# Kernel optimization log

Hardware: AMD Instinct MI355X
Metric: run time of the kernel (lower is better)

The kernel has to match this reference:

```python
import jax, jax.numpy as jnp
import numpy as np


def conv2d(x, w, pad=1):
    return jax.lax.conv_general_dilated(
        x, w, (1, 1), [(pad, pad), (pad, pad)],
        dimension_numbers=('NCHW', 'OIHW', 'NCHW'))


def bn(x, g, b, m, v, eps=1e-5):
    inv = g / jnp.sqrt(v + eps)
    return x * inv[None, :, None, None] + (b - m * inv)[None, :, None, None]


def deform_conv(x, wp, bp, wd):
    # v2-style DeformConv2D: internal p_conv -> offsets, bilinear sample, 3x3 conv
    b, c, h, w = x.shape
    ks = 3
    N = ks * ks
    offset = conv2d(x, wp, 1) + bp[None, :, None, None]   # (b, 2N, h, w)
    xp = jnp.pad(x, ((0, 0), (0, 0), (1, 1), (1, 1)))     # zero_padding(1)
    Hp, Wp = h + 2, w + 2
    off = offset.transpose(0, 2, 3, 1)                    # (b, h, w, 2N)
    pn_y, pn_x = jnp.meshgrid(jnp.arange(-1, 2), jnp.arange(-1, 2), indexing='ij')
    # sampling locations p = p_0 + p_n + offset (in padded coords)
    py = jnp.arange(1, h + 1)[None, :, None, None] + pn_y.reshape(-1)[None, None, None, :] + off[..., :N]
    px = jnp.arange(1, w + 1)[None, None, :, None] + pn_x.reshape(-1)[None, None, None, :] + off[..., N:]
    fy = jnp.floor(jax.lax.stop_gradient(py))
    fx = jnp.floor(jax.lax.stop_gradient(px))
    qy0 = jnp.clip(fy, 0, Hp - 1); qy1 = jnp.clip(fy + 1, 0, Hp - 1)
    qx0 = jnp.clip(fx, 0, Wp - 1); qx1 = jnp.clip(fx + 1, 0, Wp - 1)
    py = jnp.clip(py, 0, Hp - 1); px = jnp.clip(px, 0, Wp - 1)
    g_lt = (1 + (qy0 - py)) * (1 + (qx0 - px))
    g_rb = (1 - (qy1 - py)) * (1 - (qx1 - px))
    g_lb = (1 + (qy0 - py)) * (1 - (qx1 - px))
    g_rt = (1 - (qy1 - py)) * (1 + (qx0 - px))
    flat = xp.reshape(b, c, Hp * Wp)

    def gather(qy, qx):
        idx = (qy * Wp + qx).astype(jnp.int32).reshape(b, 1, -1)
        return jnp.take_along_axis(flat, idx, axis=2).reshape(b, c, h, w, N)

    x_off = (g_lt[:, None] * gather(qy0, qx0) + g_rb[:, None] * gather(qy1, qx1)
             + g_lb[:, None] * gather(qy0, qx1) + g_rt[:, None] * gather(qy1, qx0))
    outc = wd.shape[0]
    # equivalent to _reshape_x_offset + Conv2d(kernel=ks, stride=ks)
    return jnp.einsum('bchwn,ocn->bohw', x_off, wd.reshape(outc, c, N))


def setup_inputs() -> dict:
    key = jax.random.key(0)
    ks = jax.random.split(key, 24)
    B, H, W = 256, 28, 28

    def nrm(k, s, sc=1.0):
        return jax.random.normal(k, s, jnp.float32) * sc

    return {
        'x': nrm(ks[0], (B, 3, H, W)),
        'w1': nrm(ks[1], (32, 3, 3, 3), 0.2),
        'g1': jax.random.uniform(ks[2], (32,), jnp.float32) + 0.5,
        'b1': nrm(ks[3], (32,), 0.1),
        'm1': nrm(ks[4], (32,), 0.1),
        'v1': jax.random.uniform(ks[5], (32,), jnp.float32) + 0.5,
        'wp': nrm(ks[6], (18, 32, 3, 3), 0.01),  # p_conv: small offsets
        'bp': nrm(ks[7], (18,), 0.1),
        'w2': nrm(ks[8], (32, 32, 3, 3), 0.1),
        'g2': jax.random.uniform(ks[9], (32,), jnp.float32) + 0.5,
        'b2': nrm(ks[10], (32,), 0.1),
        'm2': nrm(ks[11], (32,), 0.1),
        'v2': jax.random.uniform(ks[12], (32,), jnp.float32) + 0.5,
        'w3': nrm(ks[13], (64, 32, 3, 3), 0.1),
        'g3': jax.random.uniform(ks[14], (64,), jnp.float32) + 0.5,
        'b3': nrm(ks[15], (64,), 0.1),
        'm3': nrm(ks[16], (64,), 0.1),
        'v3': jax.random.uniform(ks[17], (64,), jnp.float32) + 0.5,
        'wc': nrm(ks[18], (10, 64), 0.1),
        'bc': nrm(ks[19], (10,), 0.1),
    }


def reference(x, w1, g1, b1, m1, v1, wp, bp, w2, g2, b2, m2, v2,
              w3, g3, b3, m3, v3, wc, bc):
    h = bn(jax.nn.relu(conv2d(x, w1)), g1, b1, m1, v1)
    h = bn(jax.nn.relu(deform_conv(h, wp, bp, w2)), g2, b2, m2, v2)
    h = bn(jax.nn.relu(conv2d(h, w3)), g3, b3, m3, v3)
    h = h.mean(axis=(2, 3))               # avg_pool2d(28) on 28x28 -> global mean
    logits = h @ wc.T + bc
    return jax.nn.log_softmax(logits, axis=1)
```

## Files before the change

### kernel.cpp

```cpp
#include <hip/hip_runtime.h>
#include <hip/hip_bf16.h>
#include <math.h>

typedef __attribute__((ext_vector_type(8))) short short8;
typedef __attribute__((ext_vector_type(8))) _Float16 half8;
typedef __attribute__((ext_vector_type(4))) float floatx4;

#define NB 256
#define NW 16
#define NT (NW * 64)

#define WPB_OFF 0u
#define W2B_OFF 18432u
#define W3B_OFF 36864u
#define W1B_OFF 73728u
#define C1S_OFF 75776u
#define C2S_OFF 75904u
#define C3S_OFF 76032u

#define L_IMG1 0
#define L_U    50240
#define L_OFFT 100480
#define L_WL   125056
#define L_TOT  162944

static __device__ __forceinline__ unsigned short f2h(float f) {
    _Float16 h = (_Float16)f;
    unsigned short u;
    __builtin_memcpy(&u, &h, 2);
    return u;
}
static __device__ __forceinline__ float h2f(unsigned short u) {
    _Float16 h;
    __builtin_memcpy(&h, &u, 2);
    return (float)h;
}

static __device__ __forceinline__ unsigned pkh(float a, float b) {
    _Float16 ha = (_Float16)a, hb = (_Float16)b;
    unsigned short ua, ub;
    __builtin_memcpy(&ua, &ha, 2);
    __builtin_memcpy(&ub, &hb, 2);
    return (unsigned)ua | ((unsigned)ub << 16);
}

static __device__ __forceinline__ half8 h8(uint4 u) {
    half8 r;
    __builtin_memcpy(&r, &u, 16);
    return r;
}

static __device__ __forceinline__ unsigned pkmul_l(unsigned a, unsigned b) {
    unsigned d;
    asm("v_pk_mul_f16 %0, %1, %2 op_sel:[0,0] op_sel_hi:[0,1]"
        : "=v"(d) : "v"(a), "v"(b));
    return d;
}
static __device__ __forceinline__ unsigned pkfma_l(unsigned a, unsigned b, unsigned c) {
    unsigned d;
    asm("v_pk_fma_f16 %0, %1, %2, %3 op_sel:[0,0,0] op_sel_hi:[0,1,1]"
        : "=v"(d) : "v"(a), "v"(b), "v"(c));
    return d;
}
static __device__ __forceinline__ unsigned pkfma_h(unsigned a, unsigned b, unsigned c) {
    unsigned d;
    asm("v_pk_fma_f16 %0, %1, %2, %3 op_sel:[1,0,0] op_sel_hi:[1,1,1]"
        : "=v"(d) : "v"(a), "v"(b), "v"(c));
    return d;
}

__global__ void wcvt(const float* __restrict__ wp, const float* __restrict__ w2,
                     const float* __restrict__ w3, const float* __restrict__ w1,
                     const float* __restrict__ g1, const float* __restrict__ b1,
                     const float* __restrict__ m1, const float* __restrict__ v1,
                     const float* __restrict__ g2, const float* __restrict__ b2,
                     const float* __restrict__ m2, const float* __restrict__ v2,
                     const float* __restrict__ g3, const float* __restrict__ b3,
                     const float* __restrict__ m3, const float* __restrict__ v3,
                     unsigned short* __restrict__ wpb, unsigned short* __restrict__ w2b,
                     unsigned short* __restrict__ w3b, unsigned short* __restrict__ w1b,
                     float* __restrict__ c1s, float* __restrict__ c2s,
                     float* __restrict__ c3s)
{
    int t = blockIdx.x * 256 + threadIdx.x;
    if (t < 9216) {
        int oc = t / 288, k = t % 288;
        int n = k >> 5, ic = k & 31;
        wpb[t] = (oc < 18) ? f2h(wp[oc * 288 + ic * 9 + n]) : (unsigned short)0;
    } else if (t < 18432) {
        int i = t - 9216;
        int oc = i / 288, k = i % 288;
        int n = k >> 5, ic = k & 31;
        float inv = g2[oc] * rsqrtf(v2[oc] + 1e-5f);
        w2b[i] = f2h(w2[oc * 288 + ic * 9 + n] * inv);
    } else if (t < 36864) {
        int i = t - 18432;
        int oc = i / 288, k = i % 288;
        int n = k >> 5, ic = k & 31;
        float inv = g3[oc] * rsqrtf(v3[oc] + 1e-5f);
        w3b[i] = f2h(w3[oc * 288 + ic * 9 + n] * inv);
    } else if (t < 37888) {
        int i = t - 36864;
        int oc = i >> 5, k = i & 31;
        int n = k / 3, ic = k - n * 3;
        float inv = g1[oc] * rsqrtf(v1[oc] + 1e-5f);
        w1b[i] = (k < 27) ? f2h(w1[oc * 27 + ic * 9 + n] * inv) : (unsigned short)0;
    } else if (t < 37920) {
        int c = t - 37888;
        float inv = g1[c] * rsqrtf(v1[c] + 1e-5f);
        c1s[c] = b1[c] - m1[c] * inv;
    } else if (t < 37952) {
        int c = t - 37920;
        float inv = g2[c] * rsqrtf(v2[c] + 1e-5f);
        c2s[c] = b2[c] - m2[c] * inv;
    } else if (t < 38016) {
        int c = t - 37952;
        float inv = g3[c] * rsqrtf(v3[c] + 1e-5f);
        c3s[c] = b3[c] - m3[c] * inv;
    }
}

__global__ __launch_bounds__(NT, 4) void meganet(
    const float* __restrict__ x,
    const unsigned short* __restrict__ wpb, const unsigned short* __restrict__ w2b,
    const unsigned short* __restrict__ w3b, const unsigned short* __restrict__ w1b,
    const float* __restrict__ c1s, const float* __restrict__ c2s,
    const float* __restrict__ c3s, const float* __restrict__ bp,
    const float* __restrict__ wc, const float* __restrict__ bc,
    float* __restrict__ outp)
{
    __shared__ __align__(16) unsigned char ALL[L_TOT];
    int t = threadIdx.x, b = blockIdx.x;
    int w = t >> 6, l = t & 63, col = l & 15, q = l >> 4;

    unsigned char* img1 = ALL + L_IMG1;
    unsigned char* uimg = ALL + L_U;

    {
        const float4* xg = (const float4*)(x + (size_t)b * 2352);
        float4* xl = (float4*)uimg;
        for (int i = t; i < 588; i += NT) xl[i] = xg[i];
    }
    {
        const uint4* s1 = (const uint4*)wpb;
        const uint4* s2 = (const uint4*)w2b;
        for (int i = t; i < 2304; i += NT) {
            int row = i / 36, g = i - row * 36;
            uint4 v = (row < 32) ? s1[row * 36 + g] : s2[(row - 32) * 36 + g];
            *(uint4*)(ALL + L_WL + row * 592 + g * 16) = v;
        }
        if (t < 128) *(uint4*)(ALL + L_OFFT + t * 16) = ((const uint4*)w1b)[t];
    }
    if (t == 700) ((float*)uimg)[2352] = 0.f;
    if (t < 4)  *(uint4*)(img1 + 784 * 64 + t * 16) = make_uint4(0u, 0u, 0u, 0u);
    if (t >= 4 && t < 8) *(uint4*)(uimg + 784 * 64 + (t - 4) * 16) = make_uint4(0u, 0u, 0u, 0u);

    float s0 = c1s[col], s1v = c1s[16 + col];
    float bias0 = bp[col];
    float bias1 = (col < 2) ? bp[16 + col] : 0.f;
    float sh0 = c2s[col], sh1 = c2s[16 + col];

    __syncthreads();

    {
        half8 bf0 = h8(*(const uint4*)(ALL + L_OFFT + col * 64 + q * 16));
        half8 bf1 = h8(*(const uint4*)(ALL + L_OFFT + (16 + col) * 64 + q * 16));
        const float* xs = (const float*)uimg;
        for (int mt = w; mt < 49; mt += NW) {
            int p = mt * 16 + col;
            int y = p / 28, xx = p % 28;
            unsigned au[4];
#pragma unroll
            for (int jp = 0; jp < 4; jp++) {
                float vv[2];
#pragma unroll
                for (int h = 0; h < 2; h++) {
                    int k = q * 8 + jp * 2 + h;
                    int n = k / 3, ic = k - n * 3;
                    int yy = y + n / 3 - 1, xc = xx + n % 3 - 1;
                    bool ok = (k < 27) && ((unsigned)yy < 28u) && ((unsigned)xc < 28u);
                    int idx = ok ? (ic * 784 + yy * 28 + xc) : 2352;
                    vv[h] = xs[idx];
                }
                au[jp] = pkh(vv[0], vv[1]);
            }
            uint4 a4 = make_uint4(au[0], au[1], au[2], au[3]);
            half8 a = h8(a4);
            floatx4 d0 = {0.f, 0.f, 0.f, 0.f}, d1 = {0.f, 0.f, 0.f, 0.f};
            d0 = __builtin_amdgcn_mfma_f32_16x16x32_f16(a, bf0, d0, 0, 0, 0);
            d1 = __builtin_amdgcn_mfma_f32_16x16x32_f16(a, bf1, d1, 0, 0, 0);
#pragma unroll
            for (int r = 0; r < 4; r++) {
                int pout = mt * 16 + q * 4 + r;
                *(unsigned short*)(img1 + pout * 64 + col * 2) = f2h(fmaxf(d0[r], 0.f) + s0);
                *(unsigned short*)(img1 + pout * 64 + 32 + col * 2) = f2h(fmaxf(d1[r], 0.f) + s1v);
            }
        }
    }
    __syncthreads();

    {
        const unsigned char* ib = img1;
        unsigned char* wsc = ALL + L_OFFT + w * 1536;
        unsigned short* otw = (unsigned short*)wsc;
        unsigned char* gscr = wsc + 576;

        half8 b2fr[18];
#pragma unroll
        for (int n = 0; n < 9; n++) {
            b2fr[n]     = h8(*(const uint4*)(ALL + L_WL + (32 + col) * 592 + n * 64 + q * 16));
            b2fr[9 + n] = h8(*(const uint4*)(ALL + L_WL + (48 + col) * 592 + n * 64 + q * 16));
        }

        for (int mt = w; mt < 49; mt += NW) {
            int p = mt * 16 + col;
            int y = p / 28, xx = p % 28;

            floatx4 a0 = {0.f, 0.f, 0.f, 0.f}, a1 = {0.f, 0.f, 0.f, 0.f};
#pragma unroll
            for (int n = 0; n < 9; n++) {
                int yy = y + n / 3 - 1, xc = xx + n % 3 - 1;
                bool ok = ((unsigned)yy < 28u) && ((unsigned)xc < 28u);
                int tp = ok ? (yy * 28 + xc) : 784;
                half8 a  = h8(*(const uint4*)(ib + tp * 64 + q * 16));
                half8 p0 = h8(*(const uint4*)(ALL + L_WL + col * 592 + n * 64 + q * 16));
                half8 p1 = h8(*(const uint4*)(ALL + L_WL + (16 + col) * 592 + n * 64 + q * 16));
                a0 = __builtin_amdgcn_mfma_f32_16x16x32_f16(a, p0, a0, 0, 0, 0);
                a1 = __builtin_amdgcn_mfma_f32_16x16x32_f16(a, p1, a1, 0, 0, 0);
            }
#pragma unroll
            for (int r = 0; r < 4; r++)
                otw[(q * 4 + r) * 18 + col] = f2h(a0[r] + bias0);
            if (col < 2) {
#pragma unroll
                for (int r = 0; r < 4; r++)
                    otw[(q * 4 + r) * 18 + 16 + col] = f2h(a1[r] + bias1);
            }
            __asm__ volatile("s_waitcnt lgkmcnt(0)" ::: "memory");

            floatx4 d0 = {0.f, 0.f, 0.f, 0.f}, d1 = {0.f, 0.f, 0.f, 0.f};
#pragma unroll
            for (int tg = 0; tg < 3; tg++) {
                if (l < 48) {
                    int px = l & 15, n = tg * 3 + (l >> 4);
                    int pg = mt * 16 + px;
                    int yg = pg / 28, xg = pg % 28;
                    float offy = h2f(otw[px * 18 + n]);
                    float offx = h2f(otw[px * 18 + 9 + n]);
                    float py = (float)(yg + n / 3) + offy;
                    float pxf = (float)(xg + n % 3) + offx;
                    float fy = floorf(py), fx = floorf(pxf);
                    float qy0 = fminf(fmaxf(fy, 0.f), 29.f);
                    float qy1 = fminf(fmaxf(fy + 1.f, 0.f), 29.f);
                    float qx0 = fminf(fmaxf(fx, 0.f), 29.f);
                    float qx1 = fminf(fmaxf(fx + 1.f, 0.f), 29.f);
                    float pyc = fminf(fmaxf(py, 0.f), 29.f);
                    float pxc = fminf(fmaxf(pxf, 0.f), 29.f);
                    float glt = (1.f + (qy0 - pyc)) * (1.f + (qx0 - pxc));
                    float grb = (1.f - (qy1 - pyc)) * (1.f - (qx1 - pxc));
                    float glb = (1.f + (qy0 - pyc)) * (1.f - (qx1 - pxc));
                    float grt = (1.f - (qy1 - pyc)) * (1.f + (qx0 - pxc));
                    int iy0 = (int)qy0, iy1 = (int)qy1, ix0 = (int)qx0, ix1 = (int)qx1;
                    int ly0 = iy0 - 1, ly1 = iy1 - 1, lx0 = ix0 - 1, lx1 = ix1 - 1;
                    bool v00 = ((unsigned)ly0 < 28u) && ((unsigned)lx0 < 28u);
                    bool v11 = ((unsigned)ly1 < 28u) && ((unsigned)lx1 < 28u);
                    bool v01 = ((unsigned)ly0 < 28u) && ((unsigned)lx1 < 28u);
                    bool v10 = ((unsigned)ly1 < 28u) && ((unsigned)lx0 < 28u);
                    unsigned p00 = v00 ? (unsigned)(ly0 * 28 + lx0) : 784u;
                    unsigned p11 = v11 ? (unsigned)(ly1 * 28 + lx1) : 784u;
                    unsigned p01 = v01 ? (unsigned)(ly0 * 28 + lx1) : 784u;
                    unsigned p10 = v10 ? (unsigned)(ly1 * 28 + lx0) : 784u;
                    uint4 rec = make_uint4(pkh(glt, grb), pkh(glb, grt),
                                           p00 | (p11 << 16), p01 | (p10 << 16));
                    *(uint4*)(gscr + l * 16) = rec;
                }
                __asm__ volatile("s_waitcnt lgkmcnt(0)" ::: "memory");

#pragma unroll
                for (int k3 = 0; k3 < 3; k3++) {
                    int n = tg * 3 + k3;
                    uint4 rec = *(const uint4*)(gscr + (k3 * 16 + col) * 16);
                    int p00 = (int)(rec.z & 0xffffu), p11 = (int)(rec.z >> 16);
                    int p01 = (int)(rec.w & 0xffffu), p10 = (int)(rec.w >> 16);
                    uint4 u00 = *(const uint4*)(ib + p00 * 64 + q * 16);
                    uint4 u11 = *(const uint4*)(ib + p11 * 64 + q * 16);
                    uint4 u01 = *(const uint4*)(ib + p01 * 64 + q * 16);
                    uint4 u10 = *(const uint4*)(ib + p10 * 64 + q * 16);
                    unsigned f0 = pkfma_h(rec.y, u10.x,
                                  pkfma_l(rec.y, u01.x,
                                  pkfma_h(rec.x, u11.x,
                                  pkmul_l(rec.x, u00.x))));
                    unsigned f1 = pkfma_h(rec.y, u10.y,
                                  pkfma_l(rec.y, u01.y,
                                  pkfma_h(rec.x, u11.y,
                                  pkmul_l(rec.x, u00.y))));
                    unsigned f2 = pkfma_h(rec.y, u10.z,
                                  pkfma_l(rec.y, u01.z,
                                  pkfma_h(rec.x, u11.z,
                                  pkmul_l(rec.x, u00.z))));
                    unsigned f3 = pkfma_h(rec.y, u10.w,
                                  pkfma_l(rec.y, u01.w,
                                  pkfma_h(rec.x, u11.w,
                                  pkmul_l(rec.x, u00.w))));
                    uint4 af4 = make_uint4(f0, f1, f2, f3);
                    half8 af = h8(af4);
                    d0 = __builtin_amdgcn_mfma_f32_16x16x32_f16(af, b2fr[n], d0, 0, 0, 0);
                    d1 = __builtin_amdgcn_mfma_f32_16x16x32_f16(af, b2fr[9 + n], d1, 0, 0, 0);
                }
            }
#pragma unroll
            for (int r = 0; r < 4; r++) {
                int pout = mt * 16 + q * 4 + r;
                *(unsigned short*)(uimg + pout * 64 + col * 2) = f2h(fmaxf(d0[r], 0.f) + sh0);
                *(unsigned short*)(uimg + pout * 64 + 32 + col * 2) = f2h(fmaxf(d1[r], 0.f) + sh1);
            }
        }
    }
    __syncthreads();

    {
        const uint4* src = (const uint4*)w3b;
        for (int i = t; i < 2304; i += NT) {
            int row = i / 36, g = i - row * 36;
            *(uint4*)(ALL + L_WL + row * 592 + g * 16) = src[row * 36 + g];
        }
    }
    __syncthreads();

    {
        float* part = (float*)(ALL + L_OFFT);
        int ocp = w & 1;
        const unsigned char* ib = uimg;

        half8 wfr[18];
#pragma unroll
        for (int n = 0; n < 9; n++) {
            wfr[n]     = h8(*(const uint4*)(ALL + L_WL + (ocp * 32 + col) * 592 + n * 64 + q * 16));
            wfr[9 + n] = h8(*(const uint4*)(ALL + L_WL + (ocp * 32 + 16 + col) * 592 + n * 64 + q * 16));
        }

        float psA = 0.f, psB = 0.f;
        for (int mt = (w >> 1); mt < 49; mt += (NW / 2)) {
            int p = mt * 16 + col;
            int y = p / 28, xx = p % 28;
            floatx4 cA = {0.f, 0.f, 0.f, 0.f}, cB = {0.f, 0.f, 0.f, 0.f};
#pragma unroll
            for (int n = 0; n < 9; n++) {
                int yy = y + n / 3 - 1, xc = xx + n % 3 - 1;
                bool ok = ((unsigned)yy < 28u) && ((unsigned)xc < 28u);
                int tp = ok ? (yy * 28 + xc) : 784;
                half8 a = h8(*(const uint4*)(ib + tp * 64 + q * 16));
                cA = __builtin_amdgcn_mfma_f32_16x16x32_f16(a, wfr[n], cA, 0, 0, 0);
                cB = __builtin_amdgcn_mfma_f32_16x16x32_f16(a, wfr[9 + n], cB, 0, 0, 0);
            }
            psA += fmaxf(cA[0], 0.f) + fmaxf(cA[1], 0.f) + fmaxf(cA[2], 0.f) + fmaxf(cA[3], 0.f);
            psB += fmaxf(cB[0], 0.f) + fmaxf(cB[1], 0.f) + fmaxf(cB[2], 0.f) + fmaxf(cB[3], 0.f);
        }
        psA += __shfl_xor(psA, 16, 64); psA += __shfl_xor(psA, 32, 64);
        psB += __shfl_xor(psB, 16, 64); psB += __shfl_xor(psB, 32, 64);
        if (l < 16) { part[w * 32 + l] = psA; part[w * 32 + 16 + l] = psB; }
    }
    __syncthreads();

    if (t < 64) {
        const float* part = (const float*)(ALL + L_OFFT);
        int hi = t >> 5, c = t & 31;
        float s = 0.f;
#pragma unroll
        for (int j = 0; j < NW / 2; j++) s += part[(2 * j + hi) * 32 + c];
        float feat = s * (1.f / 784.f) + c3s[t];
        float lg[10];
        float mx = -1e30f;
#pragma unroll
        for (int j = 0; j < 10; j++) {
            float v = feat * wc[j * 64 + t];
            v += __shfl_xor(v, 1, 64);  v += __shfl_xor(v, 2, 64);
            v += __shfl_xor(v, 4, 64);  v += __shfl_xor(v, 8, 64);
            v += __shfl_xor(v, 16, 64); v += __shfl_xor(v, 32, 64);
            lg[j] = v + bc[j];
            mx = fmaxf(mx, lg[j]);
        }
        float se = 0.f;
#pragma unroll
        for (int j = 0; j < 10; j++) se += expf(lg[j] - mx);
        float lse = logf(se);
#pragma unroll
        for (int j = 0; j < 10; j++)
            if (t == j) outp[(size_t)b * 10 + j] = lg[j] - mx - lse;
    }
}

extern "C" void kernel_launch(void* const* d_in, const int* in_sizes, int n_in,
                              void* d_out, int out_size, void* d_ws, size_t ws_size,
                              hipStream_t stream)
{
    (void)in_sizes; (void)n_in; (void)out_size; (void)ws_size;
    const float* x  = (const float*)d_in[0];
    const float* w1 = (const float*)d_in[1];
    const float* g1 = (const float*)d_in[2];
    const float* b1 = (const float*)d_in[3];
    const float* m1 = (const float*)d_in[4];
    const float* v1 = (const float*)d_in[5];
    const float* wp = (const float*)d_in[6];
    const float* bp = (const float*)d_in[7];
    const float* w2 = (const float*)d_in[8];
    const float* g2 = (const float*)d_in[9];
    const float* b2 = (const float*)d_in[10];
    const float* m2 = (const float*)d_in[11];
    const float* v2 = (const float*)d_in[12];
    const float* w3 = (const float*)d_in[13];
    const float* g3 = (const float*)d_in[14];
    const float* b3 = (const float*)d_in[15];
    const float* m3 = (const float*)d_in[16];
    const float* v3 = (const float*)d_in[17];
    const float* wc = (const float*)d_in[18];
    const float* bc = (const float*)d_in[19];
    float* outp = (float*)d_out;

    unsigned char* ws = (unsigned char*)d_ws;
    unsigned short* wpb = (unsigned short*)(ws + WPB_OFF);
    unsigned short* w2b = (unsigned short*)(ws + W2B_OFF);
    unsigned short* w3b = (unsigned short*)(ws + W3B_OFF);
    unsigned short* w1b = (unsigned short*)(ws + W1B_OFF);
    float* c1s = (float*)(ws + C1S_OFF);
    float* c2s = (float*)(ws + C2S_OFF);
    float* c3s = (float*)(ws + C3S_OFF);

    wcvt<<<149, 256, 0, stream>>>(wp, w2, w3, w1, g1, b1, m1, v1,
                                  g2, b2, m2, v2, g3, b3, m3, v3,
                                  wpb, w2b, w3b, w1b, c1s, c2s, c3s);
    meganet<<<NB, NT, 0, stream>>>(x, wpb, w2b, w3b, w1b, c1s, c2s, c3s,
                                   bp, wc, bc, outp);
}
```

Measured before the change: 131.1 us.

## Exchange bilinear sample records via ds_bpermute and cut block to 12 waves

The per-wave sampling records (packed bilinear weights and pixel indices) used to go through an LDS scratch store, a waitcnt and an LDS reload. They are now passed across lanes in registers with ds_bpermute. Pixel indices are pre-shifted into byte offsets to save address arithmetic. The block also drops from 16 to 12 waves with launch bounds of 3, which changes occupancy and how many tiles each wave handles per stage.

```diff
diff --git a/kernel.cpp b/kernel.cpp
--- a/kernel.cpp
+++ b/kernel.cpp
@@ -7,7 +7,7 @@
 typedef __attribute__((ext_vector_type(4))) float floatx4;
 
 #define NB 256
-#define NW 16
+#define NW 12
 #define NT (NW * 64)
 
 #define WPB_OFF 0u
@@ -120,7 +120,7 @@
     }
 }
 
-__global__ __launch_bounds__(NT, 4) void meganet(
+__global__ __launch_bounds__(NT, 3) void meganet(
     const float* __restrict__ x,
     const unsigned short* __restrict__ wpb, const unsigned short* __restrict__ w2b,
     const unsigned short* __restrict__ w3b, const unsigned short* __restrict__ w1b,
@@ -201,9 +201,7 @@
 
     {
         const unsigned char* ib = img1;
-        unsigned char* wsc = ALL + L_OFFT + w * 1536;
-        unsigned short* otw = (unsigned short*)wsc;
-        unsigned char* gscr = wsc + 576;
+        unsigned short* otw = (unsigned short*)(ALL + L_OFFT + w * 1536);
 
         half8 b2fr[18];
 #pragma unroll
@@ -211,6 +209,9 @@
             b2fr[n]     = h8(*(const uint4*)(ALL + L_WL + (32 + col) * 592 + n * 64 + q * 16));
             b2fr[9 + n] = h8(*(const uint4*)(ALL + L_WL + (48 + col) * 592 + n * 64 + q * 16));
         }
+
+        int colb4 = col * 4;
+        const unsigned char* ibq = ib + q * 16;
 
         for (int mt = w; mt < 49; mt += NW) {
             int p = mt * 16 + col;
@@ -241,6 +242,7 @@
             floatx4 d0 = {0.f, 0.f, 0.f, 0.f}, d1 = {0.f, 0.f, 0.f, 0.f};
 #pragma unroll
             for (int tg = 0; tg < 3; tg++) {
+                unsigned r0 = 0, r1 = 0, r2 = 0, r3 = 0;
                 if (l < 48) {
                     int px = l & 15, n = tg * 3 + (l >> 4);
                     int pg = mt * 16 + px;
@@ -270,38 +272,40 @@
                     unsigned p11 = v11 ? (unsigned)(ly1 * 28 + lx1) : 784u;
                     unsigned p01 = v01 ? (unsigned)(ly0 * 28 + lx1) : 784u;
                     unsigned p10 = v10 ? (unsigned)(ly1 * 28 + lx0) : 784u;
-                    uint4 rec = make_uint4(pkh(glt, grb), pkh(glb, grt),
-                                           p00 | (p11 << 16), p01 | (p10 << 16));
-                    *(uint4*)(gscr + l * 16) = rec;
+                    r0 = pkh(glt, grb);
+                    r1 = pkh(glb, grt);
+                    r2 = (p00 << 6) | (p11 << 22);
+                    r3 = (p01 << 6) | (p10 << 22);
                 }
-                __asm__ volatile("s_waitcnt lgkmcnt(0)" ::: "memory");
 
 #pragma unroll
                 for (int k3 = 0; k3 < 3; k3++) {
                     int n = tg * 3 + k3;
-                    uint4 rec = *(const uint4*)(gscr + (k3 * 16 + col) * 16);
-                    int p00 = (int)(rec.z & 0xffffu), p11 = (int)(rec.z >> 16);
-                    int p01 = (int)(rec.w & 0xffffu), p10 = (int)(rec.w >> 16);
-                    uint4 u00 = *(const uint4*)(ib + p00 * 64 + q * 16);
-                    uint4 u11 = *(const uint4*)(ib + p11 * 64 + q * 16);
-                    uint4 u01 = *(const uint4*)(ib + p01 * 64 + q * 16);
-                    uint4 u10 = *(const uint4*)(ib + p10 * 64 + q * 16);
-                    unsigned f0 = pkfma_h(rec.y, u10.x,
-                                  pkfma_l(rec.y, u01.x,
-                                  pkfma_h(rec.x, u11.x,
-                                  pkmul_l(rec.x, u00.x))));
-                    unsigned f1 = pkfma_h(rec.y, u10.y,
-                                  pkfma_l(rec.y, u01.y,
-                                  pkfma_h(rec.x, u11.y,
-                                  pkmul_l(rec.x, u00.y))));
-                    unsigned f2 = pkfma_h(rec.y, u10.z,
-                                  pkfma_l(rec.y, u01.z,
-                                  pkfma_h(rec.x, u11.z,
-                                  pkmul_l(rec.x, u00.z))));
-                    unsigned f3 = pkfma_h(rec.y, u10.w,
-                                  pkfma_l(rec.y, u01.w,
-                                  pkfma_h(rec.x, u11.w,
-                                  pkmul_l(rec.x, u00.w))));
+                    int srcb = colb4 + k3 * 64;
+                    unsigned gA = (unsigned)__builtin_amdgcn_ds_bpermute(srcb, (int)r0);
+                    unsigned gB = (unsigned)__builtin_amdgcn_ds_bpermute(srcb, (int)r1);
+                    unsigned iA = (unsigned)__builtin_amdgcn_ds_bpermute(srcb, (int)r2);
+                    unsigned iB = (unsigned)__builtin_amdgcn_ds_bpermute(srcb, (int)r3);
+                    uint4 u00 = *(const uint4*)(ibq + (iA & 0xffffu));
+                    uint4 u11 = *(const uint4*)(ibq + (iA >> 16));
+                    uint4 u01 = *(const uint4*)(ibq + (iB & 0xffffu));
+                    uint4 u10 = *(const uint4*)(ibq + (iB >> 16));
+                    unsigned f0 = pkfma_h(gB, u10.x,
+                                  pkfma_l(gB, u01.x,
+                                  pkfma_h(gA, u11.x,
+                                  pkmul_l(gA, u00.x))));
+                    unsigned f1 = pkfma_h(gB, u10.y,
+                                  pkfma_l(gB, u01.y,
+                                  pkfma_h(gA, u11.y,
+                                  pkmul_l(gA, u00.y))));
+                    unsigned f2 = pkfma_h(gB, u10.z,
+                                  pkfma_l(gB, u01.z,
+                                  pkfma_h(gA, u11.z,
+                                  pkmul_l(gA, u00.z))));
+                    unsigned f3 = pkfma_h(gB, u10.w,
+                                  pkfma_l(gB, u01.w,
+                                  pkfma_h(gA, u11.w,
+                                  pkmul_l(gA, u00.w))));
                     uint4 af4 = make_uint4(f0, f1, f2, f3);
                     half8 af = h8(af4);
                     d0 = __builtin_amdgcn_mfma_f32_16x16x32_f16(af, b2fr[n], d0, 0, 0, 0);
```

Result: faster. 127.7 us (-2.6%).

## XOR-swizzle fp16 activation layout in LDS and shrink workgroup to 12 waves

Applied to the files above, without the earlier changes.

Activation images in LDS (64 bytes per pixel) now use an XOR swizzle of the 16-byte chunk index, keyed on pixel bits, on both the write and read side, including the precomputed bilinear gather offsets. The goal is fewer LDS bank conflicts on the 16-byte MFMA operand loads and scattered stores. The workgroup also drops from 16 to 12 waves, with launch bounds adjusted to match. Fewer waves means less latency hiding, and the NW-dependent loop partitioning must still cover all tiles, which it appears to do.

```diff
diff --git a/kernel.cpp b/kernel.cpp
--- a/kernel.cpp
+++ b/kernel.cpp
@@ -7,7 +7,7 @@
 typedef __attribute__((ext_vector_type(4))) float floatx4;
 
 #define NB 256
-#define NW 16
+#define NW 12
 #define NT (NW * 64)
 
 #define WPB_OFF 0u
@@ -23,6 +23,7 @@
 #define L_OFFT 100480
 #define L_WL   125056
 #define L_TOT  162944
+
 
 static __device__ __forceinline__ unsigned short f2h(float f) {
     _Float16 h = (_Float16)f;
@@ -120,7 +121,7 @@
     }
 }
 
-__global__ __launch_bounds__(NT, 4) void meganet(
+__global__ __launch_bounds__(NT, 3) void meganet(
     const float* __restrict__ x,
     const unsigned short* __restrict__ wpb, const unsigned short* __restrict__ w2b,
     const unsigned short* __restrict__ w3b, const unsigned short* __restrict__ w1b,
@@ -132,6 +133,9 @@
     __shared__ __align__(16) unsigned char ALL[L_TOT];
     int t = threadIdx.x, b = blockIdx.x;
     int w = t >> 6, l = t & 63, col = l & 15, q = l >> 4;
+    int qs = q << 4;
+    int chxA = ((col >> 3) << 4) | ((col & 7) * 2);
+    int chxB = ((((16 + col) >> 3) & 3) << 4) | ((col & 7) * 2);
 
     unsigned char* img1 = ALL + L_IMG1;
     unsigned char* uimg = ALL + L_U;
@@ -192,8 +196,9 @@
 #pragma unroll
             for (int r = 0; r < 4; r++) {
                 int pout = mt * 16 + q * 4 + r;
-                *(unsigned short*)(img1 + pout * 64 + col * 2) = f2h(fmaxf(d0[r], 0.f) + s0);
-                *(unsigned short*)(img1 + pout * 64 + 32 + col * 2) = f2h(fmaxf(d1[r], 0.f) + s1v);
+                int sp = (pout << 6) | ((pout & 6) << 3);
+                *(unsigned short*)(img1 + (sp ^ chxA)) = f2h(fmaxf(d0[r], 0.f) + s0);
+                *(unsigned short*)(img1 + (sp ^ chxB)) = f2h(fmaxf(d1[r], 0.f) + s1v);
             }
         }
     }
@@ -222,7 +227,8 @@
                 int yy = y + n / 3 - 1, xc = xx + n % 3 - 1;
                 bool ok = ((unsigned)yy < 28u) && ((unsigned)xc < 28u);
                 int tp = ok ? (yy * 28 + xc) : 784;
-                half8 a  = h8(*(const uint4*)(ib + tp * 64 + q * 16));
+                int sp = (tp << 6) | ((tp & 6) << 3);
+                half8 a  = h8(*(const uint4*)(ib + (sp ^ qs)));
                 half8 p0 = h8(*(const uint4*)(ALL + L_WL + col * 592 + n * 64 + q * 16));
                 half8 p1 = h8(*(const uint4*)(ALL + L_WL + (16 + col) * 592 + n * 64 + q * 16));
                 a0 = __builtin_amdgcn_mfma_f32_16x16x32_f16(a, p0, a0, 0, 0, 0);
@@ -270,8 +276,12 @@
                     unsigned p11 = v11 ? (unsigned)(ly1 * 28 + lx1) : 784u;
                     unsigned p01 = v01 ? (unsigned)(ly0 * 28 + lx1) : 784u;
                     unsigned p10 = v10 ? (unsigned)(ly1 * 28 + lx0) : 784u;
+                    unsigned s00 = (p00 << 6) | ((p00 & 6u) << 3);
+                    unsigned s11 = (p11 << 6) | ((p11 & 6u) << 3);
+                    unsigned s01 = (p01 << 6) | ((p01 & 6u) << 3);
+                    unsigned s10 = (p10 << 6) | ((p10 & 6u) << 3);
                     uint4 rec = make_uint4(pkh(glt, grb), pkh(glb, grt),
-                                           p00 | (p11 << 16), p01 | (p10 << 16));
+                                           s00 | (s11 << 16), s01 | (s10 << 16));
                     *(uint4*)(gscr + l * 16) = rec;
                 }
                 __asm__ volatile("s_waitcnt lgkmcnt(0)" ::: "memory");
@@ -280,12 +290,12 @@
                 for (int k3 = 0; k3 < 3; k3++) {
                     int n = tg * 3 + k3;
                     uint4 rec = *(const uint4*)(gscr + (k3 * 16 + col) * 16);
-                    int p00 = (int)(rec.z & 0xffffu), p11 = (int)(rec.z >> 16);
-                    int p01 = (int)(rec.w & 0xffffu), p10 = (int)(rec.w >> 16);
-                    uint4 u00 = *(const uint4*)(ib + p00 * 64 + q * 16);
-                    uint4 u11 = *(const uint4*)(ib + p11 * 64 + q * 16);
-                    uint4 u01 = *(const uint4*)(ib + p01 * 64 + q * 16);
-                    uint4 u10 = *(const uint4*)(ib + p10 * 64 + q * 16);
+                    unsigned o00 = (rec.z & 0xffffu) ^ qs, o11 = (rec.z >> 16) ^ qs;
+                    unsigned o01 = (rec.w & 0xffffu) ^ qs, o10 = (rec.w >> 16) ^ qs;
+                    uint4 u00 = *(const uint4*)(ib + o00);
+                    uint4 u11 = *(const uint4*)(ib + o11);
+                    uint4 u01 = *(const uint4*)(ib + o01);
+                    uint4 u10 = *(const uint4*)(ib + o10);
                     unsigned f0 = pkfma_h(rec.y, u10.x,
                                   pkfma_l(rec.y, u01.x,
                                   pkfma_h(rec.x, u11.x,
@@ -311,8 +321,9 @@
 #pragma unroll
             for (int r = 0; r < 4; r++) {
                 int pout = mt * 16 + q * 4 + r;
-                *(unsigned short*)(uimg + pout * 64 + col * 2) = f2h(fmaxf(d0[r], 0.f) + sh0);
-                *(unsigned short*)(uimg + pout * 64 + 32 + col * 2) = f2h(fmaxf(d1[r], 0.f) + sh1);
+                int sp = (pout << 6) | ((pout & 6) << 3);
+                *(unsigned short*)(uimg + (sp ^ chxA)) = f2h(fmaxf(d0[r], 0.f) + sh0);
+                *(unsigned short*)(uimg + (sp ^ chxB)) = f2h(fmaxf(d1[r], 0.f) + sh1);
             }
         }
     }
@@ -349,7 +360,8 @@
                 int yy = y + n / 3 - 1, xc = xx + n % 3 - 1;
                 bool ok = ((unsigned)yy < 28u) && ((unsigned)xc < 28u);
                 int tp = ok ? (yy * 28 + xc) : 784;
-                half8 a = h8(*(const uint4*)(ib + tp * 64 + q * 16));
+                int sp = (tp << 6) | ((tp & 6) << 3);
+                half8 a = h8(*(const uint4*)(ib + (sp ^ qs)));
                 cA = __builtin_amdgcn_mfma_f32_16x16x32_f16(a, wfr[n], cA, 0, 0, 0);
                 cB = __builtin_amdgcn_mfma_f32_16x16x32_f16(a, wfr[9 + n], cB, 0, 0, 0);
             }
```

Result: faster. 125.5 us (-4.3%).
